# Performance work log

Hardware: AMD Instinct MI355X
Metric: run time of the kernel (lower is better)

The kernel has to match this reference:

```python
import jax, jax.numpy as jnp
import numpy as np
import math

N, M_KV = 8192, 8192
QDIM, KDIM, MID = 256, 256, 128
NEG_BIG = -float(1 << 32)  # matches torch.masked_fill(Attn, mask, -(1 << 32))


def setup_inputs() -> dict:
    key = jax.random.key(0)
    ks = jax.random.split(key, 8)
    main_feat = jax.random.normal(ks[0], (N, QDIM), dtype=jnp.float32)
    other_feat = jax.random.normal(ks[1], (M_KV, KDIM), dtype=jnp.float32)
    fix_feat = jax.random.uniform(ks[2], (M_KV,), dtype=jnp.float32)
    mask = jax.random.randint(ks[3], (N, M_KV), 0, 2).astype(jnp.bool_)
    # Linear params (torch.nn.Linear stores weight as [out, in])
    Wq = jax.random.normal(ks[4], (MID, QDIM), dtype=jnp.float32) / math.sqrt(QDIM)
    bq = jax.random.normal(ks[5], (MID,), dtype=jnp.float32) * 0.01
    Wk = jax.random.normal(ks[6], (MID, KDIM), dtype=jnp.float32) / math.sqrt(KDIM)
    bk = jax.random.normal(ks[7], (MID,), dtype=jnp.float32) * 0.01
    return {"main_feat": main_feat, "other_feat": other_feat, "fix_feat": fix_feat,
            "mask": mask, "Wq": Wq, "bq": bq, "Wk": Wk, "bk": bk}


def reference(main_feat, other_feat, fix_feat, mask, Wq, bq, Wk, bk):
    # Projections: y = x @ W.T + b
    Q = main_feat @ Wq.T + bq            # [N, MID]
    K = other_feat @ Wk.T + bk           # [M, MID]
    scale = 1.0 / math.sqrt(MID)
    attn = jnp.einsum('nd,md->nm', Q, K) * scale   # [N, M]
    attn = jnp.where(mask, NEG_BIG, attn)
    attn = jax.nn.softmax(attn, axis=-1)
    # diag(fix_feat) @ other_feat is just a row-wise scale of V
    V = fix_feat[:, None] * other_feat   # [M, KDIM]
    return attn @ V                      # [N, KDIM]
```

## Files before the change

### kernel.cpp

```cpp
#include <hip/hip_runtime.h>
#include <hip/hip_bf16.h>
#include <stdint.h>

typedef __attribute__((ext_vector_type(8))) short short8;
typedef __attribute__((ext_vector_type(4))) float floatx4;

#define MFMA32K(a, b, c) __builtin_amdgcn_mfma_f32_16x16x32_bf16(a, b, c, 0, 0, 0)

constexpr int N_Q  = 8192;
constexpr int M_KV = 8192;
constexpr int DMID = 128;
constexpr int DV   = 256;
constexpr int MWORDS = M_KV / 64;

__device__ __forceinline__ unsigned short f2bf(float x) {
    unsigned u = __float_as_uint(x);
    u += 0x7fffu + ((u >> 16) & 1u);
    return (unsigned short)(u >> 16);
}

__device__ __forceinline__ short8 cvt_f8_bf8(float4 a, float4 b) {
    short8 r;
    r[0] = (short)f2bf(a.x); r[1] = (short)f2bf(a.y);
    r[2] = (short)f2bf(a.z); r[3] = (short)f2bf(a.w);
    r[4] = (short)f2bf(b.x); r[5] = (short)f2bf(b.y);
    r[6] = (short)f2bf(b.z); r[7] = (short)f2bf(b.w);
    return r;
}

__device__ __forceinline__ void gl_lds16(const unsigned short* g, unsigned short* l) {
    __builtin_amdgcn_global_load_lds(
        (const __attribute__((address_space(1))) unsigned int*)g,
        (__attribute__((address_space(3))) unsigned int*)l, 16, 0, 0);
}

__device__ __forceinline__ unsigned nz4(unsigned x) {
    unsigned nz = (((x & 0x7f7f7f7fu) + 0x7f7f7f7fu) | x) & 0x80808080u;
    unsigned a = (nz >> 7) & 0x01010101u;
    return (a * 0x01020408u) >> 24;
}

__device__ __forceinline__ unsigned nib4_to_16(unsigned x) {
    unsigned t = x | (x >> 4);
    return (t & 0xFFu) | ((t >> 8) & 0xFF00u);
}

__global__ __launch_bounds__(256) void pack_mask_kernel(
    const void* __restrict__ mask, unsigned long long* __restrict__ Mb)
{
    const int tid = threadIdx.x;
    const int wv = tid >> 6, lane = tid & 63;
    const int wbase = blockIdx.x * 256;

    unsigned w0 = ((const unsigned int*)mask)[lane];
    bool isf = (w0 == 0x3f800000u);
    bool isb = (w0 > 1u) && !isf;
    const int f = __ballot(isf) ? 2 : (__ballot(isb) ? 1 : 0);

    if (f == 1) {
        __shared__ unsigned short pbuf[1024];
        const uint4* g = (const uint4*)((const unsigned char*)mask + (size_t)wbase * 64);
#pragma unroll
        for (int r = 0; r < 4; ++r) {
            int p = wv * 256 + r * 64 + lane;
            uint4 v = g[p];
            unsigned m16 = nz4(v.x) | (nz4(v.y) << 4) | (nz4(v.z) << 8) | (nz4(v.w) << 12);
            pbuf[p] = (unsigned short)m16;
        }
        __syncthreads();
        Mb[wbase + tid] = ((const unsigned long long*)pbuf)[tid];
    } else {
        __shared__ unsigned char nib[4096];
        const uint4* g = (const uint4*)mask + (size_t)wbase * 16;
        uint4 v[16];
#pragma unroll
        for (int r = 0; r < 16; ++r) v[r] = g[r * 256 + tid];
#pragma unroll
        for (int r = 0; r < 16; ++r) {
            unsigned nb = (unsigned)(v[r].x != 0u)
                        | ((unsigned)(v[r].y != 0u) << 1)
                        | ((unsigned)(v[r].z != 0u) << 2)
                        | ((unsigned)(v[r].w != 0u) << 3);
            nib[r * 256 + tid] = (unsigned char)nb;
        }
        __syncthreads();
        uint4 nv = *(const uint4*)&nib[tid * 16];
        unsigned long long out =
              (unsigned long long)nib4_to_16(nv.x)
            | ((unsigned long long)nib4_to_16(nv.y) << 16)
            | ((unsigned long long)nib4_to_16(nv.z) << 32)
            | ((unsigned long long)nib4_to_16(nv.w) << 48);
        Mb[wbase + tid] = out;
    }
}

__global__ __launch_bounds__(256) void proj_kernel(
    const float* __restrict__ main_feat, const float* __restrict__ Wq, const float* __restrict__ bq,
    const float* __restrict__ other_feat, const float* __restrict__ Wk, const float* __restrict__ bk,
    unsigned short* __restrict__ Qw, unsigned short* __restrict__ Kw)
{
    const float* src;  const float* W;  const float* bias;  unsigned short* dst;
    if (blockIdx.y == 0) { src = main_feat;  W = Wq; bias = bq; dst = Qw; }
    else                 { src = other_feat; W = Wk; bias = bk; dst = Kw; }

    const int wave = threadIdx.x >> 6, lane = threadIdx.x & 63;
    const int n = lane & 15, quad = lane >> 4;
    const int row0 = blockIdx.x * 64 + wave * 16;

    short8 a[8];
    const float* ap = src + (size_t)(row0 + n) * 256 + quad * 8;
#pragma unroll
    for (int ks = 0; ks < 8; ++ks) {
        float4 x0 = *(const float4*)(ap + ks * 32);
        float4 x1 = *(const float4*)(ap + ks * 32 + 4);
        a[ks] = cvt_f8_bf8(x0, x1);
    }

    floatx4 acc[8];
#pragma unroll
    for (int nt = 0; nt < 8; ++nt) acc[nt] = floatx4{0.f, 0.f, 0.f, 0.f};

#pragma unroll
    for (int nt = 0; nt < 8; ++nt) {
        const float* wp = W + (size_t)(nt * 16 + n) * 256 + quad * 8;
#pragma unroll
        for (int ks = 0; ks < 8; ++ks) {
            float4 w0 = *(const float4*)(wp + ks * 32);
            float4 w1 = *(const float4*)(wp + ks * 32 + 4);
            short8 b = cvt_f8_bf8(w0, w1);
            acc[nt] = MFMA32K(a[ks], b, acc[nt]);
        }
    }

#pragma unroll
    for (int nt = 0; nt < 8; ++nt) {
        float bb = bias[nt * 16 + n];
#pragma unroll
        for (int reg = 0; reg < 4; ++reg) {
            int r = row0 + quad * 4 + reg;
            int c = nt * 16 + n;
            int phys = ((((c >> 3) + r) & 15) << 3) | (c & 7);
            dst[(size_t)r * DMID + phys] = f2bf(acc[nt][reg] + bb);
        }
    }
}

__global__ __launch_bounds__(256) void build_vt_kernel(
    const float* __restrict__ other_feat, const float* __restrict__ fix_feat,
    unsigned short* __restrict__ Vt)
{
    __shared__ unsigned short tile[64 * 72];
    const int t = threadIdx.x;
    const int m0 = blockIdx.x * 64, d0 = blockIdx.y * 64;

#pragma unroll
    for (int r = 0; r < 4; ++r) {
        int idx = r * 256 + t;
        int ml = idx >> 4, dl4 = (idx & 15) * 4;
        float4 v = *(const float4*)(other_feat + (size_t)(m0 + ml) * 256 + d0 + dl4);
        float f = fix_feat[m0 + ml];
        tile[(dl4 + 0) * 72 + ml] = f2bf(v.x * f);
        tile[(dl4 + 1) * 72 + ml] = f2bf(v.y * f);
        tile[(dl4 + 2) * 72 + ml] = f2bf(v.z * f);
        tile[(dl4 + 3) * 72 + ml] = f2bf(v.w * f);
    }
    __syncthreads();
#pragma unroll
    for (int r = 0; r < 8; ++r) {
        int dl = r * 8 + (t >> 5);
        int d = d0 + dl;
        int ml = (t & 31) * 2;
        int e = ml >> 5, s = (ml >> 4) & 1, q = (ml >> 2) & 3, j = ml & 3;
        int pc = e * 32 + q * 8 + s * 4 + j;
        int phys = ((((pc >> 3) + d) & 7) << 3) | (pc & 7);
        unsigned int v0 = tile[dl * 72 + ml];
        unsigned int v1 = tile[dl * 72 + ml + 1];
        *(unsigned int*)(Vt + (size_t)d * M_KV + m0 + phys) = v0 | (v1 << 16);
    }
}

__global__ __launch_bounds__(256, 2) void flash_kernel(
    const unsigned short* __restrict__ Qw, const unsigned short* __restrict__ Kw,
    const unsigned short* __restrict__ Vt, const unsigned long long* __restrict__ Mb,
    unsigned short* __restrict__ Opart, float* __restrict__ Lpart,
    int nsplit, int lgNs)
{
    __shared__ __align__(16) unsigned short k_lds[2][64 * 128];
    __shared__ __align__(16) unsigned short vt_lds[256 * 64];

    const int L = blockIdx.x + gridDim.x * blockIdx.y;
    const int ly = L & (nsplit - 1);
    const int lx = L >> lgNs;
    const int chunkLen = M_KV >> lgNs;
    const int mBeg = ly * chunkLen;
    const int tid = threadIdx.x;
    const int wave = tid >> 6, lane = tid & 63, n = lane & 15, quad = lane >> 4;
    const int qrow0 = lx * 128 + wave * 32;
    constexpr float SC = 0.08838834764831845f * 1.4426950408889634f;

    short8 qf[2][4];
#pragma unroll
    for (int qt = 0; qt < 2; ++qt)
#pragma unroll
        for (int db = 0; db < 4; ++db) {
            int row = qrow0 + qt * 16 + n;
            int phys = (db * 4 + quad + row) & 15;
            qf[qt][db] = *(const short8*)(Qw + (size_t)row * DMID + phys * 8);
        }

    floatx4 Oacc[2][16];
#pragma unroll
    for (int qt = 0; qt < 2; ++qt)
#pragma unroll
        for (int dt = 0; dt < 16; ++dt) Oacc[qt][dt] = floatx4{0.f, 0.f, 0.f, 0.f};

    float lrow[2] = {0.f, 0.f};

    const unsigned short* kg = Kw + (size_t)(wave * 4 + (lane >> 4)) * DMID + (lane & 15) * 8;
    const unsigned short* vg = Vt + (size_t)(wave * 8 + (lane >> 3)) * M_KV + (lane & 7) * 8;
    unsigned short* vld = &vt_lds[wave * 512];
    const int kqn = quad + n;

#pragma unroll
    for (int r = 0; r < 4; ++r)
        gl_lds16(kg + (size_t)(mBeg + r * 16) * DMID, &k_lds[0][wave * 512 + r * 2048]);

    const int iters = chunkLen / 64;
    for (int it = 0; it < iters; ++it) {
        const int m0 = mBeg + it * 64;
        const unsigned short* kbuf = k_lds[it & 1];

        __syncthreads();

#pragma unroll
        for (int r = 0; r < 8; ++r)
            gl_lds16(vg + (size_t)(r * 32) * M_KV + m0, vld + r * 2048);

        unsigned long long wbits[2];
#pragma unroll
        for (int qt = 0; qt < 2; ++qt)
            wbits[qt] = Mb[(size_t)(qrow0 + qt * 16 + n) * MWORDS + (m0 >> 6)];

        floatx4 ST[4][2];
#pragma unroll
        for (int kvt = 0; kvt < 4; ++kvt) {
            const int rowoff = (kvt * 16 + n) * DMID;
            short8 a0 = *(const short8*)&kbuf[rowoff + (((kqn + 0) & 15) << 3)];
            short8 a1 = *(const short8*)&kbuf[rowoff + (((kqn + 4) & 15) << 3)];
            short8 a2 = *(const short8*)&kbuf[rowoff + (((kqn + 8) & 15) << 3)];
            short8 a3 = *(const short8*)&kbuf[rowoff + (((kqn + 12) & 15) << 3)];
#pragma unroll
            for (int qt = 0; qt < 2; ++qt) {
                floatx4 s = floatx4{0.f, 0.f, 0.f, 0.f};
                s = MFMA32K(a0, qf[qt][0], s);
                s = MFMA32K(a1, qf[qt][1], s);
                s = MFMA32K(a2, qf[qt][2], s);
                s = MFMA32K(a3, qf[qt][3], s);
                ST[kvt][qt] = s;
            }
        }

        short8 pf8[2][2];
#pragma unroll
        for (int qt = 0; qt < 2; ++qt) {
            unsigned long long x = wbits[qt] >> (quad * 4);
            float lacc = 0.f;
#pragma unroll
            for (int kvt = 0; kvt < 4; ++kvt) {
                int e = kvt >> 1, s = kvt & 1;
                float p[4];
#pragma unroll
                for (int j = 0; j < 4; ++j) {
                    float v = __builtin_amdgcn_exp2f(ST[kvt][qt][j] * SC);
                    p[j] = ((x >> (kvt * 16 + j)) & 1ull) ? 0.f : v;
                    lacc += p[j];
                }
                __hip_bfloat162 h0 = __float22bfloat162_rn(make_float2(p[0], p[1]));
                __hip_bfloat162 h1 = __float22bfloat162_rn(make_float2(p[2], p[3]));
                unsigned u0, u1;
                __builtin_memcpy(&u0, &h0, 4);
                __builtin_memcpy(&u1, &h1, 4);
                ((unsigned*)&pf8[qt][e])[s * 2 + 0] = u0;
                ((unsigned*)&pf8[qt][e])[s * 2 + 1] = u1;
            }
            lrow[qt] += lacc;
        }

        __syncthreads();

        if (it + 1 < iters) {
            unsigned short* knext = (unsigned short*)&k_lds[(it + 1) & 1][wave * 512];
#pragma unroll
            for (int r = 0; r < 4; ++r)
                gl_lds16(kg + (size_t)(m0 + 64 + r * 16) * DMID, knext + r * 2048);
        }

#pragma unroll
        for (int e = 0; e < 2; ++e) {
#pragma unroll
            for (int dt = 0; dt < 16; ++dt) {
                const int vb = (dt * 16 + n) * 64 + (((e * 4 + quad + n) & 7) << 3);
                short8 bv = *(const short8*)&vt_lds[vb];
                Oacc[0][dt] = MFMA32K(pf8[0][e], bv, Oacc[0][dt]);
                Oacc[1][dt] = MFMA32K(pf8[1][e], bv, Oacc[1][dt]);
            }
        }
    }

    const size_t obase = (size_t)ly * N_Q * DV;
#pragma unroll
    for (int qt = 0; qt < 2; ++qt)
#pragma unroll
        for (int dt = 0; dt < 16; ++dt)
#pragma unroll
            for (int reg = 0; reg < 4; ++reg) {
                int gr = qrow0 + qt * 16 + quad * 4 + reg;
                Opart[obase + (size_t)gr * DV + dt * 16 + n] = f2bf(Oacc[qt][dt][reg]);
            }
#pragma unroll
    for (int qt = 0; qt < 2; ++qt) {
        float r = lrow[qt];
        r += __shfl_xor(r, 16);
        r += __shfl_xor(r, 32);
        if (quad == 0)
            Lpart[ly * N_Q + qrow0 + qt * 16 + n] = r;
    }
}

__global__ __launch_bounds__(256) void combine_kernel(
    const unsigned short* __restrict__ Opart, const float* __restrict__ Lpart,
    float* __restrict__ out, int nsplit)
{
    const int row = blockIdx.x, d = threadIdx.x;
    float L = 0.f, o = 0.f;
    for (int c = 0; c < nsplit; ++c) {
        L += Lpart[c * N_Q + row];
        unsigned int b = Opart[((size_t)c * N_Q + row) * DV + d];
        o += __uint_as_float(b << 16);
    }
    out[(size_t)row * DV + d] = o / L;
}

extern "C" void kernel_launch(void* const* d_in, const int* in_sizes, int n_in,
                              void* d_out, int out_size, void* d_ws, size_t ws_size,
                              hipStream_t stream)
{
    const float* main_feat  = (const float*)d_in[0];
    const float* other_feat = (const float*)d_in[1];
    const float* fix_feat   = (const float*)d_in[2];
    const void*  mask       = d_in[3];
    const float* Wq         = (const float*)d_in[4];
    const float* bq         = (const float*)d_in[5];
    const float* Wk         = (const float*)d_in[6];
    const float* bk         = (const float*)d_in[7];
    float* out = (float*)d_out;

    char* ws = (char*)d_ws;
    unsigned short* Qw = (unsigned short*)(ws);
    unsigned short* Kw = (unsigned short*)(ws + (1ull << 21));
    unsigned short* Vt = (unsigned short*)(ws + (2ull << 21));
    unsigned long long* Mb = (unsigned long long*)(ws + (8ull << 20) + 1024);
    float* Lpart = (float*)(ws + (16ull << 20) + 2048);

    const size_t base = (16ull << 20) + 2048;
    auto need = [&](int ns) {
        return base + (size_t)ns * N_Q * 4 + (size_t)ns * N_Q * DV * 2;
    };
    int nsplit = 1, lgNs = 0;
    if (ws_size >= need(8))      { nsplit = 8; lgNs = 3; }
    else if (ws_size >= need(4)) { nsplit = 4; lgNs = 2; }
    else if (ws_size >= need(2)) { nsplit = 2; lgNs = 1; }

    unsigned short* Opart = (unsigned short*)(Lpart + (size_t)nsplit * N_Q);

    hipLaunchKernelGGL(pack_mask_kernel, dim3(N_Q * MWORDS / 256), dim3(256), 0, stream,
                       mask, Mb);
    hipLaunchKernelGGL(proj_kernel, dim3(128, 2), dim3(256), 0, stream,
                       main_feat, Wq, bq, other_feat, Wk, bk, Qw, Kw);
    hipLaunchKernelGGL(build_vt_kernel, dim3(128, 4), dim3(256), 0, stream,
                       other_feat, fix_feat, Vt);
    hipLaunchKernelGGL(flash_kernel, dim3(64, nsplit), dim3(256), 0, stream,
                       Qw, Kw, Vt, Mb, Opart, Lpart, nsplit, lgNs);
    hipLaunchKernelGGL(combine_kernel, dim3(N_Q), dim3(256), 0, stream,
                       Opart, Lpart, out, nsplit);
}
```

Before: 474.6 us.

## Fuse mask bit-packing into flash kernel and prefetch raw mask per tile

```diff
diff --git a/kernel.cpp b/kernel.cpp
--- a/kernel.cpp
+++ b/kernel.cpp
@@ -11,7 +11,6 @@
 constexpr int M_KV = 8192;
 constexpr int DMID = 128;
 constexpr int DV   = 256;
-constexpr int MWORDS = M_KV / 64;
 
 __device__ __forceinline__ unsigned short f2bf(float x) {
     unsigned u = __float_as_uint(x);
@@ -38,60 +37,6 @@
     unsigned nz = (((x & 0x7f7f7f7fu) + 0x7f7f7f7fu) | x) & 0x80808080u;
     unsigned a = (nz >> 7) & 0x01010101u;
     return (a * 0x01020408u) >> 24;
-}
-
-__device__ __forceinline__ unsigned nib4_to_16(unsigned x) {
-    unsigned t = x | (x >> 4);
-    return (t & 0xFFu) | ((t >> 8) & 0xFF00u);
-}
-
-__global__ __launch_bounds__(256) void pack_mask_kernel(
-    const void* __restrict__ mask, unsigned long long* __restrict__ Mb)
-{
-    const int tid = threadIdx.x;
-    const int wv = tid >> 6, lane = tid & 63;
-    const int wbase = blockIdx.x * 256;
-
-    unsigned w0 = ((const unsigned int*)mask)[lane];
-    bool isf = (w0 == 0x3f800000u);
-    bool isb = (w0 > 1u) && !isf;
-    const int f = __ballot(isf) ? 2 : (__ballot(isb) ? 1 : 0);
-
-    if (f == 1) {
-        __shared__ unsigned short pbuf[1024];
-        const uint4* g = (const uint4*)((const unsigned char*)mask + (size_t)wbase * 64);
-#pragma unroll
-        for (int r = 0; r < 4; ++r) {
-            int p = wv * 256 + r * 64 + lane;
-            uint4 v = g[p];
-            unsigned m16 = nz4(v.x) | (nz4(v.y) << 4) | (nz4(v.z) << 8) | (nz4(v.w) << 12);
-            pbuf[p] = (unsigned short)m16;
-        }
-        __syncthreads();
-        Mb[wbase + tid] = ((const unsigned long long*)pbuf)[tid];
-    } else {
-        __shared__ unsigned char nib[4096];
-        const uint4* g = (const uint4*)mask + (size_t)wbase * 16;
-        uint4 v[16];
-#pragma unroll
-        for (int r = 0; r < 16; ++r) v[r] = g[r * 256 + tid];
-#pragma unroll
-        for (int r = 0; r < 16; ++r) {
-            unsigned nb = (unsigned)(v[r].x != 0u)
-                        | ((unsigned)(v[r].y != 0u) << 1)
-                        | ((unsigned)(v[r].z != 0u) << 2)
-                        | ((unsigned)(v[r].w != 0u) << 3);
-            nib[r * 256 + tid] = (unsigned char)nb;
-        }
-        __syncthreads();
-        uint4 nv = *(const uint4*)&nib[tid * 16];
-        unsigned long long out =
-              (unsigned long long)nib4_to_16(nv.x)
-            | ((unsigned long long)nib4_to_16(nv.y) << 16)
-            | ((unsigned long long)nib4_to_16(nv.z) << 32)
-            | ((unsigned long long)nib4_to_16(nv.w) << 48);
-        Mb[wbase + tid] = out;
-    }
 }
 
 __global__ __launch_bounds__(256) void proj_kernel(
@@ -179,15 +124,14 @@
     }
 }
 
-__global__ __launch_bounds__(256, 2) void flash_kernel(
+template<int ESZ>
+__device__ __forceinline__ void flash_body(
     const unsigned short* __restrict__ Qw, const unsigned short* __restrict__ Kw,
-    const unsigned short* __restrict__ Vt, const unsigned long long* __restrict__ Mb,
+    const unsigned short* __restrict__ Vt, const unsigned int* __restrict__ mask,
     unsigned short* __restrict__ Opart, float* __restrict__ Lpart,
-    int nsplit, int lgNs)
-{
-    __shared__ __align__(16) unsigned short k_lds[2][64 * 128];
-    __shared__ __align__(16) unsigned short vt_lds[256 * 64];
-
+    int nsplit, int lgNs,
+    unsigned short* k_lds , unsigned short* vt_lds )
+{
     const int L = blockIdx.x + gridDim.x * blockIdx.y;
     const int ly = L & (nsplit - 1);
     const int lx = L >> lgNs;
@@ -221,14 +165,36 @@
     unsigned short* vld = &vt_lds[wave * 512];
     const int kqn = quad + n;
 
+    uint4    mv4[2][4];
+    unsigned mv1[2][4];
+
+    auto load_mask = [&](int m0l) {
+#pragma unroll
+        for (int qt = 0; qt < 2; ++qt) {
+            const size_t row = (size_t)(qrow0 + qt * 16 + n);
+            if constexpr (ESZ == 4) {
+                const unsigned* mp = mask + row * M_KV + m0l + quad * 4;
+#pragma unroll
+                for (int kvt = 0; kvt < 4; ++kvt)
+                    mv4[qt][kvt] = *(const uint4*)(mp + kvt * 16);
+            } else {
+                const unsigned* mp = mask + row * (M_KV / 4) + (m0l >> 2) + quad;
+#pragma unroll
+                for (int kvt = 0; kvt < 4; ++kvt)
+                    mv1[qt][kvt] = mp[kvt * 4];
+            }
+        }
+    };
+
 #pragma unroll
     for (int r = 0; r < 4; ++r)
-        gl_lds16(kg + (size_t)(mBeg + r * 16) * DMID, &k_lds[0][wave * 512 + r * 2048]);
+        gl_lds16(kg + (size_t)(mBeg + r * 16) * DMID, &k_lds[wave * 512 + r * 2048]);
+    load_mask(mBeg);
 
     const int iters = chunkLen / 64;
     for (int it = 0; it < iters; ++it) {
         const int m0 = mBeg + it * 64;
-        const unsigned short* kbuf = k_lds[it & 1];
+        const unsigned short* kbuf = k_lds + (it & 1) * 8192;
 
         __syncthreads();
 
@@ -236,12 +202,28 @@
         for (int r = 0; r < 8; ++r)
             gl_lds16(vg + (size_t)(r * 32) * M_KV + m0, vld + r * 2048);
 
-        unsigned long long wbits[2];
-#pragma unroll
-        for (int qt = 0; qt < 2; ++qt)
-            wbits[qt] = Mb[(size_t)(qrow0 + qt * 16 + n) * MWORDS + (m0 >> 6)];
+        unsigned wq[2];
+#pragma unroll
+        for (int qt = 0; qt < 2; ++qt) {
+            unsigned b = 0;
+            if constexpr (ESZ == 4) {
+#pragma unroll
+                for (int kvt = 0; kvt < 4; ++kvt) {
+                    const unsigned* c = (const unsigned*)&mv4[qt][kvt];
+#pragma unroll
+                    for (int j = 0; j < 4; ++j)
+                        b |= (c[j] != 0u ? 1u : 0u) << (kvt * 4 + j);
+                }
+            } else {
+#pragma unroll
+                for (int kvt = 0; kvt < 4; ++kvt)
+                    b |= nz4(mv1[qt][kvt]) << (kvt * 4);
+            }
+            wq[qt] = b;
+        }
 
         floatx4 ST[4][2];
+        __builtin_amdgcn_s_setprio(1);
 #pragma unroll
         for (int kvt = 0; kvt < 4; ++kvt) {
             const int rowoff = (kvt * 16 + n) * DMID;
@@ -259,11 +241,12 @@
                 ST[kvt][qt] = s;
             }
         }
+        __builtin_amdgcn_s_setprio(0);
 
         short8 pf8[2][2];
 #pragma unroll
         for (int qt = 0; qt < 2; ++qt) {
-            unsigned long long x = wbits[qt] >> (quad * 4);
+            const unsigned x = wq[qt];
             float lacc = 0.f;
 #pragma unroll
             for (int kvt = 0; kvt < 4; ++kvt) {
@@ -272,7 +255,7 @@
 #pragma unroll
                 for (int j = 0; j < 4; ++j) {
                     float v = __builtin_amdgcn_exp2f(ST[kvt][qt][j] * SC);
-                    p[j] = ((x >> (kvt * 16 + j)) & 1ull) ? 0.f : v;
+                    p[j] = ((x >> (kvt * 4 + j)) & 1u) ? 0.f : v;
                     lacc += p[j];
                 }
                 __hip_bfloat162 h0 = __float22bfloat162_rn(make_float2(p[0], p[1]));
@@ -289,12 +272,14 @@
         __syncthreads();
 
         if (it + 1 < iters) {
-            unsigned short* knext = (unsigned short*)&k_lds[(it + 1) & 1][wave * 512];
+            unsigned short* knext = k_lds + ((it + 1) & 1) * 8192 + wave * 512;
 #pragma unroll
             for (int r = 0; r < 4; ++r)
                 gl_lds16(kg + (size_t)(m0 + 64 + r * 16) * DMID, knext + r * 2048);
-        }
-
+            load_mask(m0 + 64);
+        }
+
+        __builtin_amdgcn_s_setprio(1);
 #pragma unroll
         for (int e = 0; e < 2; ++e) {
 #pragma unroll
@@ -305,6 +290,7 @@
                 Oacc[1][dt] = MFMA32K(pf8[1][e], bv, Oacc[1][dt]);
             }
         }
+        __builtin_amdgcn_s_setprio(0);
     }
 
     const size_t obase = (size_t)ly * N_Q * DV;
@@ -325,6 +311,28 @@
         if (quad == 0)
             Lpart[ly * N_Q + qrow0 + qt * 16 + n] = r;
     }
+}
+
+__global__ __launch_bounds__(256, 2) void flash_kernel(
+    const unsigned short* __restrict__ Qw, const unsigned short* __restrict__ Kw,
+    const unsigned short* __restrict__ Vt, const unsigned int* __restrict__ mask,
+    unsigned short* __restrict__ Opart, float* __restrict__ Lpart,
+    int nsplit, int lgNs)
+{
+    __shared__ __align__(16) unsigned short k_lds[2][64 * 128];
+    __shared__ __align__(16) unsigned short vt_lds[256 * 64];
+
+    unsigned w0 = mask[threadIdx.x & 63];
+    bool isf = (w0 == 0x3f800000u);
+    bool isb = (w0 > 1u) && !isf;
+    bool wide = (__ballot(isf) != 0ull) || (__ballot(isb) == 0ull);
+
+    if (wide)
+        flash_body<4>(Qw, Kw, Vt, mask, Opart, Lpart, nsplit, lgNs,
+                      &k_lds[0][0], vt_lds);
+    else
+        flash_body<1>(Qw, Kw, Vt, mask, Opart, Lpart, nsplit, lgNs,
+                      &k_lds[0][0], vt_lds);
 }
 
 __global__ __launch_bounds__(256) void combine_kernel(
@@ -359,7 +367,6 @@
     unsigned short* Qw = (unsigned short*)(ws);
     unsigned short* Kw = (unsigned short*)(ws + (1ull << 21));
     unsigned short* Vt = (unsigned short*)(ws + (2ull << 21));
-    unsigned long long* Mb = (unsigned long long*)(ws + (8ull << 20) + 1024);
     float* Lpart = (float*)(ws + (16ull << 20) + 2048);
 
     const size_t base = (16ull << 20) + 2048;
@@ -373,14 +380,12 @@
 
     unsigned short* Opart = (unsigned short*)(Lpart + (size_t)nsplit * N_Q);
 
-    hipLaunchKernelGGL(pack_mask_kernel, dim3(N_Q * MWORDS / 256), dim3(256), 0, stream,
-                       mask, Mb);
     hipLaunchKernelGGL(proj_kernel, dim3(128, 2), dim3(256), 0, stream,
                        main_feat, Wq, bq, other_feat, Wk, bk, Qw, Kw);
     hipLaunchKernelGGL(build_vt_kernel, dim3(128, 4), dim3(256), 0, stream,
                        other_feat, fix_feat, Vt);
     hipLaunchKernelGGL(flash_kernel, dim3(64, nsplit), dim3(256), 0, stream,
-                       Qw, Kw, Vt, Mb, Opart, Lpart, nsplit, lgNs);
+                       Qw, Kw, Vt, (const unsigned int*)mask, Opart, Lpart, nsplit, lgNs);
     hipLaunchKernelGGL(combine_kernel, dim3(N_Q), dim3(256), 0, stream,
                        Opart, Lpart, out, nsplit);
 }
```

Result: no change. 471.8 us (-0.6%).
